# Kernel optimization log

Hardware: AMD Instinct MI355X
Metric: run time of the kernel (lower is better)

## Reference

```python
import math
import jax, jax.numpy as jnp
import numpy as np

N_HEAD = 32
HEAD_DIM = 64
ROTARY_DIM = 32
ROTARY_BASE = 10000.0


def _rope(u, cos, sin):
    # u: [B, S, H, head_dim]; cos/sin: [S, ROTARY_DIM//2]
    u_rot = u[..., :ROTARY_DIM].astype(jnp.float32)
    u1, u2 = jnp.split(u_rot, 2, axis=-1)          # [B,S,H,rot/2] each
    c = cos[None, :, None, :]
    s = sin[None, :, None, :]
    r = jnp.concatenate([u1 * c - u2 * s, u1 * s + u2 * c], axis=-1).astype(u.dtype)
    return jnp.concatenate([r, u[..., ROTARY_DIM:]], axis=-1)


def setup_inputs() -> dict:
    key = jax.random.key(0)
    ks = jax.random.split(key, 5)
    B, S, D = 2, 2048, 2048
    std = 1.0 / math.sqrt(D)
    x = jax.random.normal(ks[0], (B, S, D), dtype=jnp.float32)
    Wqkv = jax.random.normal(ks[1], (D, 3 * D), dtype=jnp.float32) * std
    b_qkv = jax.random.normal(ks[2], (3 * D,), dtype=jnp.float32) * 0.01
    Wout = jax.random.normal(ks[3], (D, D), dtype=jnp.float32) * std
    b_out = jax.random.normal(ks[4], (D,), dtype=jnp.float32) * 0.01
    return {"x": x, "Wqkv": Wqkv, "b_qkv": b_qkv, "Wout": Wout, "b_out": b_out}


def reference(x, Wqkv, b_qkv, Wout, b_out):
    B, S, D = x.shape
    H, hd = N_HEAD, HEAD_DIM
    # QKV projection -> [B, S, 3, H, hd]
    qkv = (x @ Wqkv + b_qkv).reshape(B, S, 3, H, hd)
    # Rotary cos/sin cache (fp32 position indices, as in the module)
    inv_freq = 1.0 / (ROTARY_BASE ** (jnp.arange(0, ROTARY_DIM, 2, dtype=jnp.float32) / ROTARY_DIM))
    t = jnp.arange(S, dtype=jnp.float32)
    freqs = jnp.outer(t, inv_freq)                 # [S, ROTARY_DIM//2]
    cos, sin = jnp.cos(freqs), jnp.sin(freqs)
    q = _rope(qkv[:, :, 0], cos, sin)
    k = _rope(qkv[:, :, 1], cos, sin)
    v = qkv[:, :, 2]
    scale = 1.0 / math.sqrt(hd)
    scores = jnp.einsum('bthd,bshd->bhts', q, k * scale)   # [B,H,S,S]
    rows = jnp.arange(S)[:, None]
    cols = jnp.arange(S)[None, :]
    causal_mask = cols > rows                      # seqlen_k == seqlen_q here
    scores = jnp.where(causal_mask[None, None], jnp.asarray(-10000.0, scores.dtype), scores)
    attn = jax.nn.softmax(scores, axis=-1)         # dropout p=0.0
    out = jnp.einsum('bhts,bshd->bthd', attn, v).reshape(B, S, D)
    return out @ Wout + b_out
```

## Files before the change

kernel.cpp:

```cpp
#include <hip/hip_runtime.h>
#include <stdint.h>
#include <math.h>

#define DEV static __device__ __forceinline__

typedef __attribute__((ext_vector_type(8))) short bf16x8;
typedef __attribute__((ext_vector_type(4))) float f32x4;
typedef __attribute__((ext_vector_type(8))) unsigned short u16x8;
typedef __attribute__((ext_vector_type(4))) unsigned short u16x4;
typedef __attribute__((ext_vector_type(2))) unsigned int u32x2;

enum { B_ = 2, S_ = 2048, D_ = 2048, H_ = 32, HD_ = 64, N3_ = 6144, M_ = 4096 };

DEV unsigned short f2bf(float f) {
  unsigned u = __float_as_uint(f);
  u += 0x7FFFu + ((u >> 16) & 1u);
  return (unsigned short)(u >> 16);
}
DEV float bf2f(unsigned short s) { return __uint_as_float(((unsigned)s) << 16); }

DEV void load16(const void* g, void* l) {
  __builtin_amdgcn_global_load_lds((const __attribute__((address_space(1))) void*)g,
                                   (__attribute__((address_space(3))) void*)l,
                                   16, 0, 0);
}

DEV f32x4 mfma16(bf16x8 a, bf16x8 b, f32x4 c) {
  return __builtin_amdgcn_mfma_f32_16x16x32_bf16(a, b, c, 0, 0, 0);
}

__global__ __launch_bounds__(256) void cvt_bf16(const float* __restrict__ in,
                                                unsigned short* __restrict__ out, int n) {
  int i = blockIdx.x * 256 + threadIdx.x;
  if (i * 8 >= n) return;
  const float4* in4 = (const float4*)in;
  float4 a = in4[i * 2 + 0];
  float4 b = in4[i * 2 + 1];
  u16x8 o;
  o[0] = f2bf(a.x); o[1] = f2bf(a.y); o[2] = f2bf(a.z); o[3] = f2bf(a.w);
  o[4] = f2bf(b.x); o[5] = f2bf(b.y); o[6] = f2bf(b.z); o[7] = f2bf(b.w);
  *(u16x8*)(out + (size_t)i * 8) = o;
}

__global__ __launch_bounds__(256) void transpose_bf16(const float* __restrict__ W,
                                                      unsigned short* __restrict__ Wt,
                                                      int Kg, int Ng) {
  __shared__ float tile[32][33];
  const int tn = blockIdx.x, tk = blockIdx.y;
  const int t = threadIdx.x;
  const int r = t >> 3, c4 = (t & 7) * 4;
  float4 v = *(const float4*)(W + (size_t)(tk * 32 + r) * Ng + tn * 32 + c4);
  tile[r][c4 + 0] = v.x; tile[r][c4 + 1] = v.y;
  tile[r][c4 + 2] = v.z; tile[r][c4 + 3] = v.w;
  __syncthreads();
  u16x4 o;
  o[0] = f2bf(tile[c4 + 0][r]);
  o[1] = f2bf(tile[c4 + 1][r]);
  o[2] = f2bf(tile[c4 + 2][r]);
  o[3] = f2bf(tile[c4 + 3][r]);
  *(u16x4*)(Wt + (size_t)(tn * 32 + r) * Kg + tk * 32 + c4) = o;
}

__global__ __launch_bounds__(256, 2) void gemm_qkv(const unsigned short* __restrict__ A,
                                                   const unsigned short* __restrict__ BT,
                                                   const float* __restrict__ bias,
                                                   unsigned short* __restrict__ Oqk,
                                                   unsigned short* __restrict__ vt,
                                                   int Mg, int Ng, int Kg) {
  __shared__ __align__(16) char lds[81920];
  const int tid = threadIdx.x;
  const int lane = tid & 63, w = tid >> 6;
  const int g = (lane >> 4) & 3, l16 = lane & 15;
  const int wn = w;

  const int wg = (blockIdx.x & 7) * (gridDim.x >> 3) + (blockIdx.x >> 3);
  const int nTM = Mg >> 7;
  const int tm = wg % nTM, tn = wg / nTM;
  const int rb = tm * 128, cb = tn * 192;
  const int NT = Kg >> 6;

  int c0, c1, c2;
  if (wn == 0)      { c0 = 0;   c1 = 16;  c2 = 32;  }
  else if (wn == 1) { c0 = 64;  c1 = 80;  c2 = 48;  }
  else if (wn == 2) { c0 = 128; c1 = 144; c2 = 96;  }
  else              { c0 = 112; c1 = 160; c2 = 176; }

  const int su0 = (g ^ (l16 & 7)) * 16;
  const int su1 = ((4 + g) ^ (l16 & 7)) * 16;
  const int offA = l16 * 128;
  const int offB0 = 16384 + (c0 + l16) * 128;
  const int offB1 = 16384 + (c1 + l16) * 128;
  const int offB2 = 16384 + (c2 + l16) * 128;

  const int r0 = tid >> 3;
  const int u8e = ((tid & 7) ^ (r0 & 7)) * 8;
  const unsigned short* sAa = A + (size_t)(rb + r0) * Kg + u8e;
  const unsigned short* sBb = BT + (size_t)(cb + r0) * Kg + u8e;
  const size_t rs32 = (size_t)Kg * 32;
  const int dstb = tid * 16;

  auto SA0 = [&](int t) { char* db = (char*)lds + ((t & 1) ? 40960 : 0);
    load16(sAa + (size_t)t * 64, db + dstb);
    load16(sAa + rs32 + (size_t)t * 64, db + 4096 + dstb); };
  auto SA1 = [&](int t) { char* db = (char*)lds + ((t & 1) ? 40960 : 0);
    load16(sAa + 2 * rs32 + (size_t)t * 64, db + 8192 + dstb);
    load16(sAa + 3 * rs32 + (size_t)t * 64, db + 12288 + dstb); };
  auto SB = [&](int t) { char* db = (char*)lds + ((t & 1) ? 40960 : 0) + 16384;
#pragma unroll
    for (int c = 0; c < 6; ++c)
      load16(sBb + c * rs32 + (size_t)t * 64, db + c * 4096 + dstb); };

  SA0(0); SA1(0); SB(0); SA0(1); SB(1);
  asm volatile("s_waitcnt vmcnt(8)" ::: "memory");
  __builtin_amdgcn_s_barrier();

  f32x4 acc[8][3] = {};
  bf16x8 a[4][2], b[3][2];

  for (int t = 0; t < NT; ++t) {
    const char* bs = (const char*)lds + ((t & 1) ? 40960 : 0);
#pragma unroll
    for (int mf = 0; mf < 4; ++mf) {
      a[mf][0] = *(const bf16x8*)(bs + offA + mf * 2048 + su0);
      a[mf][1] = *(const bf16x8*)(bs + offA + mf * 2048 + su1);
    }
    b[0][0] = *(const bf16x8*)(bs + offB0 + su0);
    b[0][1] = *(const bf16x8*)(bs + offB0 + su1);
    b[1][0] = *(const bf16x8*)(bs + offB1 + su0);
    b[1][1] = *(const bf16x8*)(bs + offB1 + su1);
    b[2][0] = *(const bf16x8*)(bs + offB2 + su0);
    b[2][1] = *(const bf16x8*)(bs + offB2 + su1);
    if (t + 1 < NT) SA1(t + 1);
    asm volatile("s_waitcnt lgkmcnt(8)" ::: "memory");
    __builtin_amdgcn_s_barrier();
    asm volatile("s_waitcnt lgkmcnt(0)" ::: "memory");
    __builtin_amdgcn_s_setprio(1);
#pragma unroll
    for (int mf = 0; mf < 4; ++mf)
#pragma unroll
      for (int nf = 0; nf < 3; ++nf)
#pragma unroll
        for (int kh = 0; kh < 2; ++kh)
          acc[mf][nf] = mfma16(a[mf][kh], b[nf][kh], acc[mf][nf]);
    __builtin_amdgcn_s_setprio(0);
    if (t == NT - 1) asm volatile("s_waitcnt vmcnt(0)" ::: "memory");
    else             asm volatile("s_waitcnt vmcnt(10)" ::: "memory");
    __builtin_amdgcn_s_barrier();
#pragma unroll
    for (int mf = 0; mf < 4; ++mf) {
      a[mf][0] = *(const bf16x8*)(bs + offA + (mf + 4) * 2048 + su0);
      a[mf][1] = *(const bf16x8*)(bs + offA + (mf + 4) * 2048 + su1);
    }
    if (t + 2 < NT) { SA0(t + 2); SB(t + 2); }
    __builtin_amdgcn_s_barrier();
    asm volatile("s_waitcnt lgkmcnt(0)" ::: "memory");
    __builtin_amdgcn_s_setprio(1);
#pragma unroll
    for (int mf = 0; mf < 4; ++mf)
#pragma unroll
      for (int nf = 0; nf < 3; ++nf)
#pragma unroll
        for (int kh = 0; kh < 2; ++kh)
          acc[mf + 4][nf] = mfma16(a[mf][kh], b[nf][kh], acc[mf + 4][nf]);
    __builtin_amdgcn_s_setprio(0);
    if (t + 2 < NT)      asm volatile("s_waitcnt vmcnt(10)" ::: "memory");
    else if (t + 1 < NT) asm volatile("s_waitcnt vmcnt(2)" ::: "memory");
    __builtin_amdgcn_s_barrier();
  }

  const int crow0 = rb + g * 4;
  const float bv0 = bias[cb + c0 + l16];
  const float bv1 = bias[cb + c1 + l16];
  const float bv2 = bias[cb + c2 + l16];
  const bool rotp = (wn < 3) && (cb + c0 < 4096);
  const float invf = exp2f(-(float)l16 * 0.83048202372184056f);

#define STOREG(NF, CG, BV) do {                                                \
    const int col0_ = cb + (CG);                                               \
    if (col0_ >= 4096) {                                                       \
      const int hv_ = (col0_ - 4096) >> 6;                                     \
      const int dd_ = (col0_ & 63) + l16;                                      \
      _Pragma("unroll")                                                        \
      for (int mf = 0; mf < 8; ++mf) {                                         \
        int rowb_ = crow0 + mf * 16;                                           \
        int bb_ = rowb_ >> 11, s0_ = rowb_ & (S_ - 1);                         \
        u16x4 ov_;                                                             \
        _Pragma("unroll")                                                      \
        for (int r = 0; r < 4; ++r) ov_[r] = f2bf(acc[mf][NF][r] + (BV));      \
        *(u16x4*)(vt + ((size_t)(bb_ * 32 + hv_) * 64 + dd_) * S_ + s0_) = ov_;\
      }                                                                        \
    } else {                                                                   \
      _Pragma("unroll")                                                        \
      for (int mf = 0; mf < 8; ++mf)                                           \
        _Pragma("unroll")                                                      \
        for (int r = 0; r < 4; ++r) {                                          \
          int row_ = crow0 + mf * 16 + r;                                      \
          Oqk[(size_t)row_ * Ng + col0_ + l16] = f2bf(acc[mf][NF][r] + (BV));  \
        }                                                                      \
    }                                                                          \
  } while (0)

  if (rotp) {
#pragma unroll
    for (int mf = 0; mf < 8; ++mf)
#pragma unroll
      for (int r = 0; r < 4; ++r) {
        int row = crow0 + mf * 16 + r;
        float v0 = acc[mf][0][r] + bv0;
        float v1 = acc[mf][1][r] + bv1;
        float ang = (float)(row & (S_ - 1)) * invf;
        float sn = __sinf(ang), cs = __cosf(ang);
        float t0 = v0 * cs - v1 * sn;
        v1 = v0 * sn + v1 * cs;
        unsigned short* p = Oqk + (size_t)row * Ng;
        p[cb + c0 + l16] = f2bf(t0);
        p[cb + c1 + l16] = f2bf(v1);
      }
  } else {
    STOREG(0, c0, bv0);
    STOREG(1, c1, bv1);
  }
  STOREG(2, c2, bv2);
#undef STOREG
}

__global__ __launch_bounds__(256, 2) void gemm_out(const unsigned short* __restrict__ A,
                                                   const unsigned short* __restrict__ BT,
                                                   const float* __restrict__ bias,
                                                   float* __restrict__ Cout,
                                                   int Mg, int Ng, int Kg) {
  __shared__ __align__(16) char lds[65536];
  const int tid = threadIdx.x;
  const int lane = tid & 63, w = tid >> 6;
  const int g = (lane >> 4) & 3, l16 = lane & 15;
  const int wn = w;

  const int wg = (blockIdx.x & 7) * (gridDim.x >> 3) + (blockIdx.x >> 3);
  const int nTM = Mg >> 7;
  const int tm = wg % nTM, tn = wg / nTM;
  const int rb = tm * 128, cb = tn * 128;
  const int NT = Kg >> 6;

  const int su0 = (g ^ (l16 & 7)) * 16;
  const int su1 = ((4 + g) ^ (l16 & 7)) * 16;
  const int offA = l16 * 128;
  const int offB0 = 16384 + (wn * 32 + l16) * 128;
  const int offB1 = offB0 + 2048;

  const int r0 = tid >> 3;
  const int u8e = ((tid & 7) ^ (r0 & 7)) * 8;
  const unsigned short* sAa = A + (size_t)(rb + r0) * Kg + u8e;
  const unsigned short* sBb = BT + (size_t)(cb + r0) * Kg + u8e;
  const size_t rs32 = (size_t)Kg * 32;
  const int dstb = tid * 16;

  auto SA0 = [&](int t) { char* db = (char*)lds + ((t & 1) ? 32768 : 0);
    load16(sAa + (size_t)t * 64, db + dstb);
    load16(sAa + rs32 + (size_t)t * 64, db + 4096 + dstb); };
  auto SA1 = [&](int t) { char* db = (char*)lds + ((t & 1) ? 32768 : 0);
    load16(sAa + 2 * rs32 + (size_t)t * 64, db + 8192 + dstb);
    load16(sAa + 3 * rs32 + (size_t)t * 64, db + 12288 + dstb); };
  auto SB = [&](int t) { char* db = (char*)lds + ((t & 1) ? 32768 : 0) + 16384;
#pragma unroll
    for (int c = 0; c < 4; ++c)
      load16(sBb + c * rs32 + (size_t)t * 64, db + c * 4096 + dstb); };

  SA0(0); SA1(0); SB(0); SA0(1); SB(1);
  asm volatile("s_waitcnt vmcnt(6)" ::: "memory");
  __builtin_amdgcn_s_barrier();

  f32x4 acc[8][2] = {};
  bf16x8 a[4][2], b[2][2];

  for (int t = 0; t < NT; ++t) {
    const char* bs = (const char*)lds + ((t & 1) ? 32768 : 0);
#pragma unroll
    for (int mf = 0; mf < 4; ++mf) {
      a[mf][0] = *(const bf16x8*)(bs + offA + mf * 2048 + su0);
      a[mf][1] = *(const bf16x8*)(bs + offA + mf * 2048 + su1);
    }
    b[0][0] = *(const bf16x8*)(bs + offB0 + su0);
    b[0][1] = *(const bf16x8*)(bs + offB0 + su1);
    b[1][0] = *(const bf16x8*)(bs + offB1 + su0);
    b[1][1] = *(const bf16x8*)(bs + offB1 + su1);
    if (t + 1 < NT) SA1(t + 1);
    asm volatile("s_waitcnt lgkmcnt(8)" ::: "memory");
    __builtin_amdgcn_s_barrier();
    asm volatile("s_waitcnt lgkmcnt(0)" ::: "memory");
    __builtin_amdgcn_s_setprio(1);
#pragma unroll
    for (int mf = 0; mf < 4; ++mf)
#pragma unroll
      for (int nf = 0; nf < 2; ++nf)
#pragma unroll
        for (int kh = 0; kh < 2; ++kh)
          acc[mf][nf] = mfma16(a[mf][kh], b[nf][kh], acc[mf][nf]);
    __builtin_amdgcn_s_setprio(0);
    if (t == NT - 1) asm volatile("s_waitcnt vmcnt(0)" ::: "memory");
    else             asm volatile("s_waitcnt vmcnt(8)" ::: "memory");
    __builtin_amdgcn_s_barrier();
#pragma unroll
    for (int mf = 0; mf < 4; ++mf) {
      a[mf][0] = *(const bf16x8*)(bs + offA + (mf + 4) * 2048 + su0);
      a[mf][1] = *(const bf16x8*)(bs + offA + (mf + 4) * 2048 + su1);
    }
    if (t + 2 < NT) { SA0(t + 2); SB(t + 2); }
    __builtin_amdgcn_s_barrier();
    asm volatile("s_waitcnt lgkmcnt(0)" ::: "memory");
    __builtin_amdgcn_s_setprio(1);
#pragma unroll
    for (int mf = 0; mf < 4; ++mf)
#pragma unroll
      for (int nf = 0; nf < 2; ++nf)
#pragma unroll
        for (int kh = 0; kh < 2; ++kh)
          acc[mf + 4][nf] = mfma16(a[mf][kh], b[nf][kh], acc[mf + 4][nf]);
    __builtin_amdgcn_s_setprio(0);
    if (t + 2 < NT)      asm volatile("s_waitcnt vmcnt(8)" ::: "memory");
    else if (t + 1 < NT) asm volatile("s_waitcnt vmcnt(2)" ::: "memory");
    __builtin_amdgcn_s_barrier();
  }

  const int crow0 = rb + g * 4;
  const int ccol0 = cb + wn * 32 + l16;
  const float bv0 = bias[ccol0];
  const float bv1 = bias[ccol0 + 16];
#pragma unroll
  for (int mf = 0; mf < 8; ++mf)
#pragma unroll
    for (int r = 0; r < 4; ++r) {
      int row = crow0 + mf * 16 + r;
      float* p = Cout + (size_t)row * Ng + ccol0;
      p[0] = acc[mf][0][r] + bv0;
      p[16] = acc[mf][1][r] + bv1;
    }
}

DEV void stage_kv(const unsigned short* __restrict__ qkv,
                  const unsigned short* __restrict__ vt,
                  unsigned char* lds, int bS, int bh64, int hoff, int kvb, int buf, int tid) {
#pragma unroll
  for (int c = 0; c < 2; ++c) {
    int p = c * 256 + tid;
    int row = p >> 3, k8 = (p & 7) ^ (row & 7);
    load16(qkv + (size_t)(bS + kvb + row) * N3_ + 2048 + hoff + 8 * k8,
           lds + buf * 8192 + p * 16);
    load16(vt + (size_t)(bh64 + row) * S_ + kvb + 8 * k8,
           lds + 16384 + buf * 8192 + p * 16);
  }
}

__global__ __launch_bounds__(256, 3) void attn_kernel(const unsigned short* __restrict__ qkv,
                                                      const unsigned short* __restrict__ vt,
                                                      unsigned short* __restrict__ ao) {
  __shared__ __align__(16) unsigned char lds[49152];
  const int tid = threadIdx.x;
  const int lane = tid & 63, wv = tid >> 6;
  const int g = lane >> 4, l16 = lane & 15;
  const int bid = blockIdx.x;
  const int qi = 15 - (bid >> 6);
  const int t6 = bid & 63;
  const int bh = ((t6 & 7) << 3) | (t6 >> 3);
  const int b = bh >> 5, h = bh & 31;
  const int qbase = qi * 128;
  const int srow0 = qbase + wv * 32;
  const int bS = b * S_, bh64 = bh * 64, hoff = h * 64;

  bf16x8 qf[2][2];
#pragma unroll
  for (int m = 0; m < 2; ++m)
#pragma unroll
    for (int kt = 0; kt < 2; ++kt)
      qf[m][kt] = *(const bf16x8*)(qkv + (size_t)(bS + srow0 + m * 16 + l16) * N3_ +
                                   hoff + kt * 32 + g * 8);

  float mrun[2] = {-INFINITY, -INFINITY}, lrun[2] = {0.f, 0.f};
  f32x4 o[2][4] = {};
  unsigned char* pw = lds + 32768 + wv * 4096;

  const int nkv = (qbase + 128) >> 6;
  stage_kv(qkv, vt, lds, bS, bh64, hoff, 0, 0, tid);
  __syncthreads();

  for (int kb = 0; kb < nkv; ++kb) {
    const int cur = kb & 1;
    if (kb + 1 < nkv) stage_kv(qkv, vt, lds, bS, bh64, hoff, (kb + 1) << 6, cur ^ 1, tid);
    const int kvb = kb << 6;
    if (kvb <= srow0 + 31) {
      const unsigned char* kbuf = lds + cur * 8192;
      const unsigned char* vbuf = lds + 16384 + cur * 8192;

      f32x4 sc[2][4];
#pragma unroll
      for (int n = 0; n < 4; ++n) {
        int row = n * 16 + l16;
        bf16x8 kf0 = *(const bf16x8*)(kbuf + (row * 8 + ((g + 0) ^ (row & 7))) * 16);
        bf16x8 kf1 = *(const bf16x8*)(kbuf + (row * 8 + ((g + 4) ^ (row & 7))) * 16);
#pragma unroll
        for (int m = 0; m < 2; ++m) {
          f32x4 z = {};
          z = mfma16(kf0, qf[m][0], z);
          z = mfma16(kf1, qf[m][1], z);
          sc[m][n] = z;
        }
      }

      const bool boundary = (kvb + 63 > srow0);
#pragma unroll
      for (int m = 0; m < 2; ++m) {
        const int qrow = srow0 + m * 16 + l16;
        if (boundary) {
#pragma unroll
          for (int n = 0; n < 4; ++n)
#pragma unroll
            for (int r = 0; r < 4; ++r) {
              int k = kvb + n * 16 + g * 4 + r;
              if (k > qrow) sc[m][n][r] = -INFINITY;
            }
        }
        float mx = fmaxf(fmaxf(sc[m][0][0], sc[m][0][1]), fmaxf(sc[m][0][2], sc[m][0][3]));
#pragma unroll
        for (int n = 1; n < 4; ++n)
          mx = fmaxf(mx, fmaxf(fmaxf(sc[m][n][0], sc[m][n][1]), fmaxf(sc[m][n][2], sc[m][n][3])));
        mx = fmaxf(mx, __shfl_xor(mx, 16));
        mx = fmaxf(mx, __shfl_xor(mx, 32));
        float pm = mx * 0.125f;
        if (!__all(pm <= mrun[m] + 8.0f)) {
          float mn = fmaxf(mrun[m], pm);
          float al = exp2f((mrun[m] - mn) * 1.44269504f);
          mrun[m] = mn; lrun[m] *= al;
#pragma unroll
          for (int d = 0; d < 4; ++d) o[m][d] *= al;
        }
        const float mt = mrun[m] * 1.44269504f;
        float p[4][4]; float rs = 0.f;
#pragma unroll
        for (int n = 0; n < 4; ++n)
#pragma unroll
          for (int r = 0; r < 4; ++r) {
            p[n][r] = exp2f(fmaf(sc[m][n][r], 0.18033688011112042f, -mt));
            rs += p[n][r];
          }
        rs += __shfl_xor(rs, 16);
        rs += __shfl_xor(rs, 32);
        lrun[m] += rs;
#pragma unroll
        for (int n = 0; n < 4; ++n) {
          unsigned lo, hi;
          asm("v_cvt_pk_bf16_f32 %0, %1, %2" : "=v"(lo) : "v"(p[n][0]), "v"(p[n][1]));
          asm("v_cvt_pk_bf16_f32 %0, %1, %2" : "=v"(hi) : "v"(p[n][2]), "v"(p[n][3]));
          int su = (n * 4 + g) ^ ((l16 & 7) << 1);
          u32x2 wq; wq[0] = lo; wq[1] = hi;
          *(u32x2*)(pw + ((m * 16 + l16) * 16 + su) * 8) = wq;
        }
      }

      bf16x8 pf[2][2];
#pragma unroll
      for (int m = 0; m < 2; ++m)
#pragma unroll
        for (int kt = 0; kt < 2; ++kt) {
          int su = (kt * 8 + g * 2) ^ ((l16 & 7) << 1);
          pf[m][kt] = *(const bf16x8*)(pw + ((m * 16 + l16) * 16 + su) * 8);
        }
#pragma unroll
      for (int dblk = 0; dblk < 4; ++dblk) {
        int row = dblk * 16 + l16;
        bf16x8 vf0 = *(const bf16x8*)(vbuf + (row * 8 + ((g + 0) ^ (row & 7))) * 16);
        bf16x8 vf1 = *(const bf16x8*)(vbuf + (row * 8 + ((g + 4) ^ (row & 7))) * 16);
#pragma unroll
        for (int m = 0; m < 2; ++m) {
          o[m][dblk] = mfma16(vf0, pf[m][0], o[m][dblk]);
          o[m][dblk] = mfma16(vf1, pf[m][1], o[m][dblk]);
        }
      }
    }
    __syncthreads();
  }

#pragma unroll
  for (int m = 0; m < 2; ++m) {
    float inv = 1.0f / lrun[m];
    int q = srow0 + m * 16 + l16;
#pragma unroll
    for (int dblk = 0; dblk < 4; ++dblk) {
      u16x4 ov;
#pragma unroll
      for (int r = 0; r < 4; ++r) ov[r] = f2bf(o[m][dblk][r] * inv);
      *(u16x4*)(ao + (size_t)(bS + q) * D_ + hoff + dblk * 16 + g * 4) = ov;
    }
  }
}

extern "C" void kernel_launch(void* const* d_in, const int* in_sizes, int n_in,
                              void* d_out, int out_size, void* d_ws, size_t ws_size,
                              hipStream_t stream) {
  const float* x = (const float*)d_in[0];
  const float* Wqkv = (const float*)d_in[1];
  const float* bqkv = (const float*)d_in[2];
  const float* Wout = (const float*)d_in[3];
  const float* bout = (const float*)d_in[4];
  float* out = (float*)d_out;

  char* ws = (char*)d_ws;
  unsigned short* Xb = (unsigned short*)(ws + 0);
  unsigned short* Wqkvt = (unsigned short*)(ws + 16777216);
  unsigned short* Woutt = (unsigned short*)(ws + 41943040);
  unsigned short* QKVb = (unsigned short*)(ws + 50331648);
  unsigned short* Vt = (unsigned short*)(ws + 100663296);
  unsigned short* AO = Xb;

  cvt_bf16<<<4096, 256, 0, stream>>>(x, Xb, M_ * D_);
  transpose_bf16<<<dim3(192, 64), 256, 0, stream>>>(Wqkv, Wqkvt, 2048, 6144);
  transpose_bf16<<<dim3(64, 64), 256, 0, stream>>>(Wout, Woutt, 2048, 2048);
  gemm_qkv<<<1024, 256, 0, stream>>>(Xb, Wqkvt, bqkv, QKVb, Vt, M_, N3_, D_);
  attn_kernel<<<1024, 256, 0, stream>>>(QKVb, Vt, AO);
  gemm_out<<<512, 256, 0, stream>>>(AO, Woutt, bout, out, M_, D_, D_);
}
```

Before: 236.3 us.

## Merge prep kernels into one launch and double attention query tile to 256

```diff
diff --git a/kernel.cpp b/kernel.cpp
--- a/kernel.cpp
+++ b/kernel.cpp
@@ -29,25 +29,9 @@
   return __builtin_amdgcn_mfma_f32_16x16x32_bf16(a, b, c, 0, 0, 0);
 }
 
-__global__ __launch_bounds__(256) void cvt_bf16(const float* __restrict__ in,
-                                                unsigned short* __restrict__ out, int n) {
-  int i = blockIdx.x * 256 + threadIdx.x;
-  if (i * 8 >= n) return;
-  const float4* in4 = (const float4*)in;
-  float4 a = in4[i * 2 + 0];
-  float4 b = in4[i * 2 + 1];
-  u16x8 o;
-  o[0] = f2bf(a.x); o[1] = f2bf(a.y); o[2] = f2bf(a.z); o[3] = f2bf(a.w);
-  o[4] = f2bf(b.x); o[5] = f2bf(b.y); o[6] = f2bf(b.z); o[7] = f2bf(b.w);
-  *(u16x8*)(out + (size_t)i * 8) = o;
-}
-
-__global__ __launch_bounds__(256) void transpose_bf16(const float* __restrict__ W,
-                                                      unsigned short* __restrict__ Wt,
-                                                      int Kg, int Ng) {
+DEV void transpose_body(const float* __restrict__ W, unsigned short* __restrict__ Wt,
+                        int Kg, int Ng, int tn, int tk, int t) {
   __shared__ float tile[32][33];
-  const int tn = blockIdx.x, tk = blockIdx.y;
-  const int t = threadIdx.x;
   const int r = t >> 3, c4 = (t & 7) * 4;
   float4 v = *(const float4*)(W + (size_t)(tk * 32 + r) * Ng + tn * 32 + c4);
   tile[r][c4 + 0] = v.x; tile[r][c4 + 1] = v.y;
@@ -59,6 +43,30 @@
   o[2] = f2bf(tile[c4 + 2][r]);
   o[3] = f2bf(tile[c4 + 3][r]);
   *(u16x4*)(Wt + (size_t)(tn * 32 + r) * Kg + tk * 32 + c4) = o;
+}
+
+__global__ __launch_bounds__(256) void prep_kernel(const float* __restrict__ x,
+                                                   const float* __restrict__ Wqkv,
+                                                   const float* __restrict__ Wout,
+                                                   unsigned short* __restrict__ Xb,
+                                                   unsigned short* __restrict__ Wqkvt,
+                                                   unsigned short* __restrict__ Woutt) {
+  const int bid = blockIdx.x, t = threadIdx.x;
+  if (bid < 12288) {
+    transpose_body(Wqkv, Wqkvt, 2048, 6144, bid % 192, bid / 192, t);
+  } else if (bid < 16384) {
+    const int r = bid - 12288;
+    transpose_body(Wout, Woutt, 2048, 2048, r & 63, r >> 6, t);
+  } else {
+    const int i = (bid - 16384) * 256 + t;
+    const float4* in4 = (const float4*)x;
+    float4 a = in4[i * 2 + 0];
+    float4 b = in4[i * 2 + 1];
+    u16x8 o;
+    o[0] = f2bf(a.x); o[1] = f2bf(a.y); o[2] = f2bf(a.z); o[3] = f2bf(a.w);
+    o[4] = f2bf(b.x); o[5] = f2bf(b.y); o[6] = f2bf(b.z); o[7] = f2bf(b.w);
+    *(u16x8*)(Xb + (size_t)i * 8) = o;
+  }
 }
 
 __global__ __launch_bounds__(256, 2) void gemm_qkv(const unsigned short* __restrict__ A,
@@ -339,30 +347,26 @@
 DEV void stage_kv(const unsigned short* __restrict__ qkv,
                   const unsigned short* __restrict__ vt,
                   unsigned char* lds, int bS, int bh64, int hoff, int kvb, int buf, int tid) {
-#pragma unroll
-  for (int c = 0; c < 2; ++c) {
-    int p = c * 256 + tid;
-    int row = p >> 3, k8 = (p & 7) ^ (row & 7);
-    load16(qkv + (size_t)(bS + kvb + row) * N3_ + 2048 + hoff + 8 * k8,
-           lds + buf * 8192 + p * 16);
-    load16(vt + (size_t)(bh64 + row) * S_ + kvb + 8 * k8,
-           lds + 16384 + buf * 8192 + p * 16);
-  }
-}
-
-__global__ __launch_bounds__(256, 3) void attn_kernel(const unsigned short* __restrict__ qkv,
+  int row = tid >> 3, k8 = (tid & 7) ^ (row & 7);
+  load16(qkv + (size_t)(bS + kvb + row) * N3_ + 2048 + hoff + 8 * k8,
+         lds + buf * 8192 + tid * 16);
+  load16(vt + (size_t)(bh64 + row) * S_ + kvb + 8 * k8,
+         lds + 16384 + buf * 8192 + tid * 16);
+}
+
+__global__ __launch_bounds__(512, 4) void attn_kernel(const unsigned short* __restrict__ qkv,
                                                       const unsigned short* __restrict__ vt,
                                                       unsigned short* __restrict__ ao) {
-  __shared__ __align__(16) unsigned char lds[49152];
+  __shared__ __align__(16) unsigned char lds[65536];
   const int tid = threadIdx.x;
   const int lane = tid & 63, wv = tid >> 6;
   const int g = lane >> 4, l16 = lane & 15;
   const int bid = blockIdx.x;
-  const int qi = 15 - (bid >> 6);
+  const int qi = 7 - (bid >> 6);
   const int t6 = bid & 63;
   const int bh = ((t6 & 7) << 3) | (t6 >> 3);
   const int b = bh >> 5, h = bh & 31;
-  const int qbase = qi * 128;
+  const int qbase = qi * 256;
   const int srow0 = qbase + wv * 32;
   const int bS = b * S_, bh64 = bh * 64, hoff = h * 64;
 
@@ -378,7 +382,7 @@
   f32x4 o[2][4] = {};
   unsigned char* pw = lds + 32768 + wv * 4096;
 
-  const int nkv = (qbase + 128) >> 6;
+  const int nkv = (qbase + 256) >> 6;
   stage_kv(qkv, vt, lds, bS, bh64, hoff, 0, 0, tid);
   __syncthreads();
 
@@ -510,10 +514,8 @@
   unsigned short* Vt = (unsigned short*)(ws + 100663296);
   unsigned short* AO = Xb;
 
-  cvt_bf16<<<4096, 256, 0, stream>>>(x, Xb, M_ * D_);
-  transpose_bf16<<<dim3(192, 64), 256, 0, stream>>>(Wqkv, Wqkvt, 2048, 6144);
-  transpose_bf16<<<dim3(64, 64), 256, 0, stream>>>(Wout, Woutt, 2048, 2048);
+  prep_kernel<<<20480, 256, 0, stream>>>(x, Wqkv, Wout, Xb, Wqkvt, Woutt);
   gemm_qkv<<<1024, 256, 0, stream>>>(Xb, Wqkvt, bqkv, QKVb, Vt, M_, N3_, D_);
-  attn_kernel<<<1024, 256, 0, stream>>>(QKVb, Vt, AO);
+  attn_kernel<<<512, 512, 0, stream>>>(QKVb, Vt, AO);
   gemm_out<<<512, 256, 0, stream>>>(AO, Woutt, bout, out, M_, D_, D_);
 }
```

Result: slower. 244.4 us (+3.4%).
